# Optimization experiments

Measured on AMD Instinct MI355X. Metric: run time of the kernel, lower is better.

The kernel has to match this reference:

```python
import jax, jax.numpy as jnp
import numpy as np

N_NODES = 100000
N_EDGES = 1600000
IN = 128
HID = 128
EPS = 1e-5


def setup_inputs() -> dict:
    key = jax.random.key(0)
    ks = jax.random.split(key, 20)
    def lin(k, fi, fo):
        return jax.random.normal(k, (fi, fo), dtype=jnp.float32) / np.sqrt(fi)
    inp = {
        'x': jax.random.normal(ks[0], (N_NODES, IN), dtype=jnp.float32),
        'src': jax.random.randint(ks[1], (N_EDGES,), 0, N_NODES),
        'dst': jax.random.randint(ks[2], (N_EDGES,), 0, N_NODES),
        # SAGEConv layer 1..3: fc_self, fc_neigh, bias
        'Wself1': lin(ks[3], IN, HID), 'Wneigh1': lin(ks[4], IN, HID), 'b1': jnp.zeros((HID,), jnp.float32),
        'Wself2': lin(ks[5], HID, HID), 'Wneigh2': lin(ks[6], HID, HID), 'b2': jnp.zeros((HID,), jnp.float32),
        'Wself3': lin(ks[7], HID, HID), 'Wneigh3': lin(ks[8], HID, HID), 'b3': jnp.zeros((HID,), jnp.float32),
        # shared BatchNorm1d(hid)
        'gamma': jnp.ones((HID,), jnp.float32), 'beta': jnp.zeros((HID,), jnp.float32),
        # decoder MLP hid->hid->hid->1
        'Wd1': lin(ks[9], HID, HID), 'bd1': jnp.zeros((HID,), jnp.float32),
        'Wd2': lin(ks[10], HID, HID), 'bd2': jnp.zeros((HID,), jnp.float32),
        'Wd3': lin(ks[11], HID, 1), 'bd3': jnp.zeros((1,), jnp.float32),
    }
    return inp


def _sage_conv(h, src, dst, deg, Wself, Wneigh, b, n):
    # mean aggregation over in-neighbors: gather + segment-sum + divide
    neigh_sum = jax.ops.segment_sum(h[src], dst, num_segments=n)  # [N, F]
    neigh_mean = neigh_sum / deg[:, None]
    return h @ Wself + neigh_mean @ Wneigh + b


def _batch_norm(h, gamma, beta):
    mu = jnp.mean(h, axis=0)
    var = jnp.mean(jnp.square(h - mu), axis=0)  # biased var, as torch BN training
    return gamma * (h - mu) * jax.lax.rsqrt(var + EPS) + beta


def reference(x, src, dst, Wself1, Wneigh1, b1, Wself2, Wneigh2, b2,
              Wself3, Wneigh3, b3, gamma, beta, Wd1, bd1, Wd2, bd2, Wd3, bd3):
    n = x.shape[0]
    deg = jax.ops.segment_sum(jnp.ones_like(dst, dtype=x.dtype), dst, num_segments=n)
    deg = jnp.maximum(deg, 1.0)
    h = _sage_conv(x, src, dst, deg, Wself1, Wneigh1, b1, n)
    h = jax.nn.relu(_batch_norm(h, gamma, beta))  # dropout = identity (eval)
    h = _sage_conv(h, src, dst, deg, Wself2, Wneigh2, b2, n)
    h = jax.nn.relu(_batch_norm(h, gamma, beta))
    h = _sage_conv(h, src, dst, deg, Wself3, Wneigh3, b3, n)
    # decoder MLP
    h = jax.nn.relu(h @ Wd1 + bd1)
    h = jax.nn.relu(h @ Wd2 + bd2)
    return h @ Wd3 + bd3  # [N, 1]
```

## Files before the change

### kernel.cpp

```cpp
#include <hip/hip_runtime.h>

typedef unsigned short u16;
typedef unsigned int u32;
using bf16x8 = __attribute__((ext_vector_type(8))) __bf16;
using f32x4  = __attribute__((ext_vector_type(4))) float;

#define CAP 48
#define LDSROW 136

__global__ void SAGE_79328045957727_kernel() {}

__device__ __forceinline__ float bf2f(u16 u) {
  union { u32 i; float f; } v; v.i = ((u32)u) << 16; return v.f;
}
__device__ __forceinline__ u16 f2bf(float f) {
  union { float f; u32 i; } v; v.f = f;
  u32 x = v.i;
  return (u16)((x + 0x7FFFu + ((x >> 16) & 1u)) >> 16);
}


__global__ void zero_kernel(int* p, int n) {
  int i = blockIdx.x * 256 + threadIdx.x;
  if (i < n) p[i] = 0;
}


__global__ __launch_bounds__(256) void build_kernel(
    const int* __restrict__ src, const int* __restrict__ dst,
    int* __restrict__ deg, int* __restrict__ csr, int E,
    const float* __restrict__ x, u16* __restrict__ xb, long nelem4,
    const float* w0, const float* w1, const float* w2, const float* w3,
    const float* w4, const float* w5, const float* w6, const float* w7,
    u16* __restrict__ wt) {
  int b = blockIdx.x;
  if (b < 1024) {
    for (int i = b * 256 + threadIdx.x; i < E; i += 1024 * 256) {
      int dv = dst[i];
      int pos = atomicAdd(&deg[dv], 1);
      if (pos < CAP) csr[(size_t)dv * CAP + pos] = src[i];
    }
  } else if (b < 1280) {
    long t = (long)(b - 1024) * 256 + threadIdx.x;
    for (long i4 = t; i4 < nelem4; i4 += 256 * 256) {
      float4 v = ((const float4*)x)[i4];
      u32* op = (u32*)(xb + i4 * 4);
      op[0] = ((u32)f2bf(v.y) << 16) | (u32)f2bf(v.x);
      op[1] = ((u32)f2bf(v.w) << 16) | (u32)f2bf(v.z);
    }
  } else {
    int tg = (b - 1280) * 256 + threadIdx.x;
    for (int k = 0; k < 8; ++k) {
      int idx = tg + k * 16384;
      int m = idx >> 14;
      int i = idx & 16383;
      const float* W = m == 0 ? w0 : m == 1 ? w1 : m == 2 ? w2 : m == 3 ? w3
                     : m == 4 ? w4 : m == 5 ? w5 : m == 6 ? w6 : w7;
      int r = i >> 7, c = i & 127;
      wt[(size_t)m * 16384 + (size_t)c * 128 + r] = f2bf(W[i]);
    }
  }
}


__global__ __launch_bounds__(256) void bnrelu_kernel(
    const u16* __restrict__ Z, u16* __restrict__ G,
    const float* __restrict__ stats, const float* __restrict__ gamma,
    const float* __restrict__ beta, long n4, float invN) {
  __shared__ float sSc[128], sSh[128];
  int t = threadIdx.x;
  if (t < 128) {
    float mu = stats[t] * invN;
    float var = stats[128 + t] * invN - mu * mu;
    float is = rsqrtf(var + 1e-5f);
    float sc = gamma[t] * is;
    sSc[t] = sc;
    sSh[t] = beta[t] - mu * sc;
  }
  __syncthreads();
  for (long i4 = (long)blockIdx.x * 256 + t; i4 < n4; i4 += (long)gridDim.x * 256) {
    uint4 q = ((const uint4*)Z)[i4];
    int c0 = ((int)(i4 & 15)) * 8;
    float e0 = fmaxf(sSc[c0+0]*bf2f((u16)(q.x & 0xffffu))+sSh[c0+0], 0.f);
    float e1 = fmaxf(sSc[c0+1]*bf2f((u16)(q.x >> 16))    +sSh[c0+1], 0.f);
    float e2 = fmaxf(sSc[c0+2]*bf2f((u16)(q.y & 0xffffu))+sSh[c0+2], 0.f);
    float e3 = fmaxf(sSc[c0+3]*bf2f((u16)(q.y >> 16))    +sSh[c0+3], 0.f);
    float e4 = fmaxf(sSc[c0+4]*bf2f((u16)(q.z & 0xffffu))+sSh[c0+4], 0.f);
    float e5 = fmaxf(sSc[c0+5]*bf2f((u16)(q.z >> 16))    +sSh[c0+5], 0.f);
    float e6 = fmaxf(sSc[c0+6]*bf2f((u16)(q.w & 0xffffu))+sSh[c0+6], 0.f);
    float e7 = fmaxf(sSc[c0+7]*bf2f((u16)(q.w >> 16))    +sSh[c0+7], 0.f);
    uint4 o;
    o.x = ((u32)f2bf(e1) << 16) | (u32)f2bf(e0);
    o.y = ((u32)f2bf(e3) << 16) | (u32)f2bf(e2);
    o.z = ((u32)f2bf(e5) << 16) | (u32)f2bf(e4);
    o.w = ((u32)f2bf(e7) << 16) | (u32)f2bf(e6);
    ((uint4*)G)[i4] = o;
  }
}


__global__ __launch_bounds__(256) void gather_kernel(
    const u16* __restrict__ G, const int* __restrict__ csr,
    const int* __restrict__ deg, u16* __restrict__ M, int N) {
  int node = blockIdx.x * 16 + (threadIdx.x >> 4);
  if (node >= N) return;
  int lane = threadIdx.x & 15;
  int fo = lane * 8;
  const int* nl = csr + (size_t)node * CAP;
  int d = deg[node];
  int dm = d < CAP ? d : CAP;
  float a0=0.f,a1=0.f,a2=0.f,a3=0.f,a4=0.f,a5=0.f,a6=0.f,a7=0.f;

#define ACC8(q) do { \
    a0 += bf2f((u16)((q).x & 0xffffu)); a1 += bf2f((u16)((q).x >> 16)); \
    a2 += bf2f((u16)((q).y & 0xffffu)); a3 += bf2f((u16)((q).y >> 16)); \
    a4 += bf2f((u16)((q).z & 0xffffu)); a5 += bf2f((u16)((q).z >> 16)); \
    a6 += bf2f((u16)((q).w & 0xffffu)); a7 += bf2f((u16)((q).w >> 16)); \
  } while (0)

  int e = 0;
  for (; e + 8 <= dm; e += 8) {
    int ia = nl[e+0], ib = nl[e+1], ic = nl[e+2], id_ = nl[e+3];
    int ie_ = nl[e+4], if_ = nl[e+5], ig = nl[e+6], ih = nl[e+7];
    uint4 q0 = *(const uint4*)(G + (size_t)ia  * 128 + fo);
    uint4 q1 = *(const uint4*)(G + (size_t)ib  * 128 + fo);
    uint4 q2 = *(const uint4*)(G + (size_t)ic  * 128 + fo);
    uint4 q3 = *(const uint4*)(G + (size_t)id_ * 128 + fo);
    uint4 q4 = *(const uint4*)(G + (size_t)ie_ * 128 + fo);
    uint4 q5 = *(const uint4*)(G + (size_t)if_ * 128 + fo);
    uint4 q6 = *(const uint4*)(G + (size_t)ig  * 128 + fo);
    uint4 q7 = *(const uint4*)(G + (size_t)ih  * 128 + fo);
    ACC8(q0); ACC8(q1); ACC8(q2); ACC8(q3);
    ACC8(q4); ACC8(q5); ACC8(q6); ACC8(q7);
  }
  if (e + 4 <= dm) {
    int ia = nl[e+0], ib = nl[e+1], ic = nl[e+2], id_ = nl[e+3];
    uint4 q0 = *(const uint4*)(G + (size_t)ia  * 128 + fo);
    uint4 q1 = *(const uint4*)(G + (size_t)ib  * 128 + fo);
    uint4 q2 = *(const uint4*)(G + (size_t)ic  * 128 + fo);
    uint4 q3 = *(const uint4*)(G + (size_t)id_ * 128 + fo);
    ACC8(q0); ACC8(q1); ACC8(q2); ACC8(q3);
    e += 4;
  }
  for (; e < dm; ++e) {
    uint4 q = *(const uint4*)(G + (size_t)nl[e] * 128 + fo);
    ACC8(q);
  }
#undef ACC8

  float inv = 1.f / (float)(d > 0 ? d : 1);
  uint4 o;
  o.x = ((u32)f2bf(a1 * inv) << 16) | (u32)f2bf(a0 * inv);
  o.y = ((u32)f2bf(a3 * inv) << 16) | (u32)f2bf(a2 * inv);
  o.z = ((u32)f2bf(a5 * inv) << 16) | (u32)f2bf(a4 * inv);
  o.w = ((u32)f2bf(a7 * inv) << 16) | (u32)f2bf(a6 * inv);
  *(uint4*)(M + (size_t)node * 128 + fo) = o;
}


__device__ __forceinline__ void stage_tile(
    const u16* __restrict__ A, u16* sT, size_t row0, int N, int tid) {
  for (int j = 0; j < 8; ++j) {
    int idx = j * 1024 + tid * 4;
    int r = idx >> 6;
    int c = idx & 63;
    size_t grow = row0 + r;
    if (grow >= (size_t)N) grow = (size_t)(N - 1);
    const u32* gp = (const u32*)(A + grow * 128) + c;
    u32 v0 = gp[0], v1 = gp[1], v2 = gp[2], v3 = gp[3];
    u32* lp = (u32*)(sT + (size_t)r * LDSROW + c * 2);
    lp[0] = v0; lp[1] = v1; lp[2] = v2; lp[3] = v3;
  }
}

__device__ __forceinline__ void preload_tile(
    const u16* __restrict__ A, u32 rb[8][4], size_t row0, int N, int tid) {
  for (int j = 0; j < 8; ++j) {
    int idx = j * 1024 + tid * 4;
    int r = idx >> 6;
    int c = idx & 63;
    size_t grow = row0 + r;
    if (grow >= (size_t)N) grow = (size_t)(N - 1);
    const u32* gp = (const u32*)(A + grow * 128) + c;
    rb[j][0] = gp[0]; rb[j][1] = gp[1]; rb[j][2] = gp[2]; rb[j][3] = gp[3];
  }
}

__device__ __forceinline__ void write_tile(
    const u32 rb[8][4], u16* sT, int tid) {
  for (int j = 0; j < 8; ++j) {
    int idx = j * 1024 + tid * 4;
    int r = idx >> 6;
    int c = idx & 63;
    u32* lp = (u32*)(sT + (size_t)r * LDSROW + c * 2);
    lp[0] = rb[j][0]; lp[1] = rb[j][1]; lp[2] = rb[j][2]; lp[3] = rb[j][3];
  }
}

__device__ __forceinline__ void mfma_tile(
    const u16* sT, const u16* __restrict__ Wt, f32x4 acc[8][2],
    int wave, int l15, int quad) {
  bf16x8 wf[2][4];
  for (int ct = 0; ct < 2; ++ct) {
    int col = wave * 32 + ct * 16 + l15;
    for (int kk = 0; kk < 4; ++kk)
      wf[ct][kk] = *(const bf16x8*)(Wt + (size_t)col * 128 + kk * 32 + quad * 8);
  }
  for (int kk = 0; kk < 4; ++kk) {
    int kbase = kk * 32 + quad * 8;
    for (int rt = 0; rt < 8; ++rt) {
      bf16x8 af = *(const bf16x8*)(sT + (size_t)(rt * 16 + l15) * LDSROW + kbase);
      acc[rt][0] = __builtin_amdgcn_mfma_f32_16x16x32_bf16(af, wf[0][kk], acc[rt][0], 0, 0, 0);
      acc[rt][1] = __builtin_amdgcn_mfma_f32_16x16x32_bf16(af, wf[1][kk], acc[rt][1], 0, 0, 0);
    }
  }
}


__global__ __launch_bounds__(256) void gemm2(
    const u16* __restrict__ A, const u16* __restrict__ B,
    const u16* __restrict__ W1t, const u16* __restrict__ W2t,
    const float* __restrict__ bias, u16* __restrict__ C,
    float* __restrict__ statsOut, int N) {
  __shared__ u16 sT[128 * LDSROW];
  int tid = threadIdx.x;
  int wave = tid >> 6;
  int lane = tid & 63;
  int l15 = lane & 15;
  int quad = lane >> 4;
  size_t row0 = (size_t)blockIdx.x * 128;

  f32x4 acc[8][2];
  for (int rt = 0; rt < 8; ++rt)
    for (int ct = 0; ct < 2; ++ct)
      for (int i = 0; i < 4; ++i) acc[rt][ct][i] = 0.f;

  u32 rb[8][4];
  preload_tile(B, rb, row0, N, tid);
  stage_tile(A, sT, row0, N, tid);
  __syncthreads();
  mfma_tile(sT, W1t, acc, wave, l15, quad);
  __syncthreads();
  write_tile(rb, sT, tid);
  __syncthreads();
  mfma_tile(sT, W2t, acc, wave, l15, quad);

  for (int ct = 0; ct < 2; ++ct) {
    int col = wave * 32 + ct * 16 + l15;
    float bv = bias[col];
    float ssum = 0.f, ssq = 0.f;
    for (int rt = 0; rt < 8; ++rt) {
      for (int i = 0; i < 4; ++i) {
        size_t row = row0 + rt * 16 + quad * 4 + i;
        if (row < (size_t)N) {
          float v = acc[rt][ct][i] + bv;
          C[row * 128 + col] = f2bf(v);
          ssum += v; ssq += v * v;
        }
      }
    }
    for (int o = 16; o < 64; o <<= 1) {
      ssum += __shfl_xor(ssum, o);
      ssq  += __shfl_xor(ssq, o);
    }
    if (quad == 0) {
      atomicAdd(&statsOut[col], ssum);
      atomicAdd(&statsOut[128 + col], ssq);
    }
  }
}


__global__ __launch_bounds__(256) void megagemm(
    const u16* __restrict__ G, const u16* __restrict__ M,
    const u16* __restrict__ wtS3, const u16* __restrict__ wtN3,
    const float* __restrict__ b3,
    const u16* __restrict__ wtD1, const float* __restrict__ bd1,
    const u16* __restrict__ wtD2, const float* __restrict__ bd2,
    const float* __restrict__ wd3, const float* __restrict__ bd3,
    float* __restrict__ outF, int N) {
  __shared__ u16 sT[128 * LDSROW];
  __shared__ float sOut[128];

  int tid = threadIdx.x;
  int wave = tid >> 6;
  int lane = tid & 63;
  int l15 = lane & 15;
  int quad = lane >> 4;
  size_t row0 = (size_t)blockIdx.x * 128;

  if (tid < 128) sOut[tid] = 0.f;

  f32x4 acc[8][2];
  for (int rt = 0; rt < 8; ++rt)
    for (int ct = 0; ct < 2; ++ct)
      for (int i = 0; i < 4; ++i) acc[rt][ct][i] = 0.f;

  u32 rb[8][4];
  preload_tile(G, rb, row0, N, tid);
  stage_tile(M, sT, row0, N, tid);
  __syncthreads();
  mfma_tile(sT, wtN3, acc, wave, l15, quad);
  __syncthreads();
  write_tile(rb, sT, tid);
  __syncthreads();
  mfma_tile(sT, wtS3, acc, wave, l15, quad);

  for (int g = 0; g < 2; ++g) {
    const u16* Wt = g ? wtD2 : wtD1;
    const float* bs = g ? bd1 : b3;
    int do_relu = g;

    __syncthreads();
    for (int ct = 0; ct < 2; ++ct) {
      int col = wave * 32 + ct * 16 + l15;
      float bv = bs[col];
      for (int rt = 0; rt < 8; ++rt) {
        for (int i = 0; i < 4; ++i) {
          int row = rt * 16 + quad * 4 + i;
          float v = acc[rt][ct][i] + bv;
          if (do_relu) v = fmaxf(v, 0.f);
          sT[(size_t)row * LDSROW + col] = f2bf(v);
        }
      }
    }
    __syncthreads();

    for (int rt = 0; rt < 8; ++rt)
      for (int ct = 0; ct < 2; ++ct)
        for (int i = 0; i < 4; ++i) acc[rt][ct][i] = 0.f;
    mfma_tile(sT, Wt, acc, wave, l15, quad);
  }

  {
    int col0 = wave * 32 + l15;
    float bv0 = bd2[col0], bv1 = bd2[col0 + 16];
    float w30 = wd3[col0], w31 = wd3[col0 + 16];
    for (int rt = 0; rt < 8; ++rt) {
      for (int i = 0; i < 4; ++i) {
        size_t row = row0 + rt * 16 + quad * 4 + i;
        float v0 = fmaxf(acc[rt][0][i] + bv0, 0.f);
        float v1 = fmaxf(acc[rt][1][i] + bv1, 0.f);
        float pv = v0 * w30 + v1 * w31;
        pv += __shfl_xor(pv, 1);
        pv += __shfl_xor(pv, 2);
        pv += __shfl_xor(pv, 4);
        pv += __shfl_xor(pv, 8);
        if (l15 == 0 && row < (size_t)N)
          atomicAdd(&sOut[rt * 16 + quad * 4 + i], pv);
      }
    }
    __syncthreads();
    if (tid < 128) {
      size_t row = row0 + tid;
      if (row < (size_t)N) outF[row] = sOut[tid] + bd3[0];
    }
  }
}


extern "C" void kernel_launch(void* const* d_in, const int* in_sizes, int n_in,
                              void* d_out, int out_size, void* d_ws, size_t ws_size,
                              hipStream_t stream) {
  const float* x      = (const float*)d_in[0];
  const int*   src    = (const int*)d_in[1];
  const int*   dst    = (const int*)d_in[2];
  const float* Wself1 = (const float*)d_in[3];
  const float* Wneigh1= (const float*)d_in[4];
  const float* b1     = (const float*)d_in[5];
  const float* Wself2 = (const float*)d_in[6];
  const float* Wneigh2= (const float*)d_in[7];
  const float* b2     = (const float*)d_in[8];
  const float* Wself3 = (const float*)d_in[9];
  const float* Wneigh3= (const float*)d_in[10];
  const float* b3     = (const float*)d_in[11];
  const float* gamma  = (const float*)d_in[12];
  const float* beta   = (const float*)d_in[13];
  const float* Wd1    = (const float*)d_in[14];
  const float* bd1    = (const float*)d_in[15];
  const float* Wd2    = (const float*)d_in[16];
  const float* bd2    = (const float*)d_in[17];
  const float* Wd3    = (const float*)d_in[18];
  const float* bd3    = (const float*)d_in[19];
  float* out = (float*)d_out;

  int N = in_sizes[0] / 128;
  int E = in_sizes[1];

  char* ws = (char*)d_ws;
  size_t off = 0;
  int* deg; int* csr; float* stats1; float* stats2;
  u16* xb; u16* ZA; u16* ZB; u16* M; u16* wt;
  deg   = (int*)(ws + off);   off += (size_t)N * 4;
  stats1= (float*)(ws + off); off += 256 * 4;
  stats2= (float*)(ws + off); off += 256 * 4;
  off = (off + 511) & ~(size_t)511;
  csr  = (int*)(ws + off);   off += ((size_t)N * CAP * 4 + 511) & ~(size_t)511;
  wt   = (u16*)(ws + off);   off += ((size_t)8 * 16384 * 2 + 511) & ~(size_t)511;
  xb   = (u16*)(ws + off);   off += ((size_t)N * 128 * 2 + 511) & ~(size_t)511;
  ZA   = (u16*)(ws + off);   off += ((size_t)N * 128 * 2 + 511) & ~(size_t)511;
  ZB   = (u16*)(ws + off);   off += ((size_t)N * 128 * 2 + 511) & ~(size_t)511;
  M    = (u16*)(ws + off);   off += ((size_t)N * 128 * 2 + 511) & ~(size_t)511;

  u16* wtS1 = wt + 0 * 16384; u16* wtN1 = wt + 1 * 16384;
  u16* wtS2 = wt + 2 * 16384; u16* wtN2 = wt + 3 * 16384;
  u16* wtS3 = wt + 4 * 16384; u16* wtN3 = wt + 5 * 16384;
  u16* wtD1 = wt + 6 * 16384; u16* wtD2 = wt + 7 * 16384;

  zero_kernel<<<(N + 512 + 255) / 256, 256, 0, stream>>>(deg, N + 512);

  long nelem4 = (long)N * 128 / 4;
  build_kernel<<<1344, 256, 0, stream>>>(
      src, dst, deg, csr, E, x, xb, nelem4,
      Wself1, Wneigh1, Wself2, Wneigh2, Wself3, Wneigh3, Wd1, Wd2, wt);

  int strips = (N + 127) / 128;
  int g16    = (N + 15) / 16;
  float invN = 1.f / (float)N;
  long n4 = (long)N * 16;

  gather_kernel<<<g16, 256, 0, stream>>>(xb, csr, deg, M, N);
  gemm2<<<strips, 256, 0, stream>>>(xb, M, wtS1, wtN1, b1, ZA, stats1, N);

  bnrelu_kernel<<<2048, 256, 0, stream>>>(ZA, ZA, stats1, gamma, beta, n4, invN);

  gather_kernel<<<g16, 256, 0, stream>>>(ZA, csr, deg, M, N);
  gemm2<<<strips, 256, 0, stream>>>(ZA, M, wtS2, wtN2, b2, ZB, stats2, N);

  bnrelu_kernel<<<2048, 256, 0, stream>>>(ZB, ZB, stats2, gamma, beta, n4, invN);

  gather_kernel<<<g16, 256, 0, stream>>>(ZB, csr, deg, M, N);
  megagemm<<<strips, 256, 0, stream>>>(
      ZB, M, wtS3, wtN3, b3, wtD1, bd1, wtD2, bd2, Wd3, bd3, out, N);
}
```

Baseline: 557.2 us.

## Partition CSR build by destination range and vectorize edge loads

The CSR build blocks are split into 8 partitions by destination node range, chosen from blockIdx mod 8. Each partition's 128 blocks scan all edges with 128-bit nontemporal loads of src/dst and only insert edges whose destination falls in their range. The aim is to keep atomics and CSR writes for a partition in a smaller region that stays cache resident, possibly local to one XCD. The cost is that each edge array is now read 8 times. The x to bf16 conversion also switches to nontemporal vector loads and stores.

```diff
diff --git a/kernel.cpp b/kernel.cpp
--- a/kernel.cpp
+++ b/kernel.cpp
@@ -4,6 +4,8 @@
 typedef unsigned int u32;
 using bf16x8 = __attribute__((ext_vector_type(8))) __bf16;
 using f32x4  = __attribute__((ext_vector_type(4))) float;
+using u32x4  = __attribute__((ext_vector_type(4))) u32;
+using u32x2  = __attribute__((ext_vector_type(2))) u32;
 
 #define CAP 48
 #define LDSROW 136
@@ -28,25 +30,44 @@
 
 __global__ __launch_bounds__(256) void build_kernel(
     const int* __restrict__ src, const int* __restrict__ dst,
-    int* __restrict__ deg, int* __restrict__ csr, int E,
+    int* __restrict__ deg, int* __restrict__ csr, int E, int npart,
     const float* __restrict__ x, u16* __restrict__ xb, long nelem4,
     const float* w0, const float* w1, const float* w2, const float* w3,
     const float* w4, const float* w5, const float* w6, const float* w7,
     u16* __restrict__ wt) {
   int b = blockIdx.x;
   if (b < 1024) {
-    for (int i = b * 256 + threadIdx.x; i < E; i += 1024 * 256) {
+    int p = b & 7;
+    int brank = b >> 3;
+    int lo = p * npart, hi = lo + npart;
+    int E4 = E >> 2;
+    for (int i = brank * 256 + threadIdx.x; i < E4; i += 128 * 256) {
+      u32x4 d4 = __builtin_nontemporal_load((const u32x4*)dst + i);
+      u32x4 s4 = __builtin_nontemporal_load((const u32x4*)src + i);
+#pragma unroll
+      for (int k = 0; k < 4; ++k) {
+        int dv = (int)d4[k];
+        if (dv >= lo && dv < hi) {
+          int pos = atomicAdd(&deg[dv], 1);
+          if (pos < CAP) csr[(size_t)dv * CAP + pos] = (int)s4[k];
+        }
+      }
+    }
+    for (int i = (E4 << 2) + brank * 256 + threadIdx.x; i < E; i += 128 * 256) {
       int dv = dst[i];
-      int pos = atomicAdd(&deg[dv], 1);
-      if (pos < CAP) csr[(size_t)dv * CAP + pos] = src[i];
+      if (dv >= lo && dv < hi) {
+        int pos = atomicAdd(&deg[dv], 1);
+        if (pos < CAP) csr[(size_t)dv * CAP + pos] = src[i];
+      }
     }
   } else if (b < 1280) {
     long t = (long)(b - 1024) * 256 + threadIdx.x;
     for (long i4 = t; i4 < nelem4; i4 += 256 * 256) {
-      float4 v = ((const float4*)x)[i4];
-      u32* op = (u32*)(xb + i4 * 4);
-      op[0] = ((u32)f2bf(v.y) << 16) | (u32)f2bf(v.x);
-      op[1] = ((u32)f2bf(v.w) << 16) | (u32)f2bf(v.z);
+      f32x4 v = __builtin_nontemporal_load((const f32x4*)x + i4);
+      u32x2 o;
+      o[0] = ((u32)f2bf(v[1]) << 16) | (u32)f2bf(v[0]);
+      o[1] = ((u32)f2bf(v[3]) << 16) | (u32)f2bf(v[2]);
+      __builtin_nontemporal_store(o, (u32x2*)(xb + i4 * 4));
     }
   } else {
     int tg = (b - 1280) * 256 + threadIdx.x;
@@ -386,6 +407,7 @@
 
   int N = in_sizes[0] / 128;
   int E = in_sizes[1];
+  int npart = (N + 7) / 8;
 
   char* ws = (char*)d_ws;
   size_t off = 0;
@@ -411,7 +433,7 @@
 
   long nelem4 = (long)N * 128 / 4;
   build_kernel<<<1344, 256, 0, stream>>>(
-      src, dst, deg, csr, E, x, xb, nelem4,
+      src, dst, deg, csr, E, npart, x, xb, nelem4,
       Wself1, Wneigh1, Wself2, Wneigh2, Wself3, Wneigh3, Wd1, Wd2, wt);
 
   int strips = (N + 127) / 128;
```

Result: faster. 523.7 us (-6.0%).
